# Kernel optimization log

Hardware: AMD Instinct MI355X
Metric: run time of the kernel (lower is better)

Reference implementation:

```python
import jax, jax.numpy as jnp
import numpy as np

DIM = 1024
NUM_HEADS = 16
HEAD_DIM = DIM // NUM_HEADS
EPS_NORM = 1e-12  # F.normalize eps
EPS_LN = 1e-5     # nn.LayerNorm eps


def setup_inputs() -> dict:
    key = jax.random.key(0)
    ks = jax.random.split(key, 6)
    x = jax.random.normal(ks[0], (4, 2048, DIM), dtype=jnp.float32)
    # LayerNorm params
    ln_w = jnp.ones((DIM,), jnp.float32)
    ln_b = jnp.zeros((DIM,), jnp.float32)
    # qkv: xavier_uniform on weight [3D, D], zero bias
    limit = float(np.sqrt(6.0 / (DIM + 3 * DIM)))
    qkv_w = jax.random.uniform(ks[1], (3 * DIM, DIM), jnp.float32, -limit, limit)
    qkv_b = jnp.zeros((3 * DIM,), jnp.float32)
    # out_proj: normal std=0.02, zero bias
    out_w = 0.02 * jax.random.normal(ks[2], (DIM, DIM), dtype=jnp.float32)
    out_b = jnp.zeros((DIM,), jnp.float32)
    return {"x": x, "ln_w": ln_w, "ln_b": ln_b, "qkv_w": qkv_w,
            "qkv_b": qkv_b, "out_w": out_w, "out_b": out_b}


def reference(x, ln_w, ln_b, qkv_w, qkv_b, out_w, out_b):
    B, N, D = x.shape
    # pre-LayerNorm
    mu = jnp.mean(x, axis=-1, keepdims=True)
    var = jnp.mean(jnp.square(x - mu), axis=-1, keepdims=True)
    h = (x - mu) / jnp.sqrt(var + EPS_LN) * ln_w + ln_b
    # QKV projection (torch Linear: y = h @ W^T + b)
    qkv = h @ qkv_w.T + qkv_b                     # [B, N, 3D]
    qkv = qkv.reshape(B, N, 3, NUM_HEADS, HEAD_DIM)
    q, k, v = (jnp.transpose(qkv[:, :, i], (0, 2, 1, 3)) for i in range(3))  # [B,H,N,hd]
    # per-head L2 normalize (F.normalize semantics: x / max(||x||, eps))
    q = q / jnp.maximum(jnp.linalg.norm(q, axis=-1, keepdims=True), EPS_NORM)
    k = k / jnp.maximum(jnp.linalg.norm(k, axis=-1, keepdims=True), EPS_NORM)
    scale = HEAD_DIM ** 0.5
    attn = jnp.einsum('bhqd,bhkd->bhqk', q, k) * scale
    attn = jax.nn.softmax(attn, axis=-1)
    out = jnp.einsum('bhqk,bhkd->bhqd', attn, v)  # [B,H,N,hd]
    out = jnp.transpose(out, (0, 2, 1, 3)).reshape(B, N, D)
    return x + out @ out_w.T + out_b
```

## Files before the change

### kernel.cpp

```cpp
#include <hip/hip_runtime.h>
#include <math.h>

constexpr int D     = 1024;
constexpr int NH    = 16;
constexpr int HD    = 64;
constexpr int SEQ   = 2048;
constexpr int BATCH = 4;
constexpr int NTOK  = BATCH * SEQ;

typedef short s16x8 __attribute__((ext_vector_type(8)));
typedef short s16x4 __attribute__((ext_vector_type(4)));
typedef float f32x4 __attribute__((ext_vector_type(4)));
typedef unsigned short u16;
typedef unsigned int   u32;

#if __has_builtin(__builtin_amdgcn_exp2f)
#define EXP2(x) __builtin_amdgcn_exp2f(x)
#else
#define EXP2(x) exp2f(x)
#endif

__device__ __forceinline__ short f2bf(float f) {
    unsigned u = __float_as_uint(f);
    unsigned r = (u + 0x7FFFu + ((u >> 16) & 1u)) >> 16;
    return (short)r;
}
__device__ __forceinline__ float bf2f(u16 s) {
    return __uint_as_float(((unsigned)s) << 16);
}

__device__ __forceinline__ u32 pack_bf16_pair(float f0, float f1) {
    u32 a = __float_as_uint(f1) + 0x8000u;
    u32 b = __float_as_uint(f0) + 0x8000u;
    return __builtin_amdgcn_perm(a, b, 0x07060302u);
}

__device__ __forceinline__ void async_lds16(const void* g, void* l) {
    __builtin_amdgcn_global_load_lds(
        (const __attribute__((address_space(1))) unsigned int*)g,
        (__attribute__((address_space(3))) unsigned int*)l, 16, 0, 0);
}

__device__ __forceinline__ float block_reduce_sum(float v, float* red) {
    int lane = threadIdx.x & 63, wid = threadIdx.x >> 6;
    #pragma unroll
    for (int off = 32; off > 0; off >>= 1) v += __shfl_down(v, off, 64);
    if (lane == 0) red[wid] = v;
    __syncthreads();
    float r = red[0] + red[1] + red[2] + red[3];
    __syncthreads();
    return r;
}

__global__ __launch_bounds__(256) void ln_kernel(const float* __restrict__ x,
                                                 const float* __restrict__ w,
                                                 const float* __restrict__ b,
                                                 u16* __restrict__ h) {
    __shared__ float red[4];
    int row = blockIdx.x;
    const float* xr = x + (size_t)row * D;
    int t = threadIdx.x;
    float v[4];
    float s = 0.f;
    #pragma unroll
    for (int i = 0; i < 4; i++) { v[i] = xr[t + 256 * i]; s += v[i]; }
    float mean = block_reduce_sum(s, red) * (1.0f / 1024.0f);
    float ss = 0.f;
    #pragma unroll
    for (int i = 0; i < 4; i++) { float d = v[i] - mean; ss += d * d; }
    float var = block_reduce_sum(ss, red) * (1.0f / 1024.0f);
    float rstd = rsqrtf(var + 1e-5f);
    u16* hr = h + (size_t)row * D;
    #pragma unroll
    for (int i = 0; i < 4; i++) {
        int c = t + 256 * i;
        hr[c] = (u16)f2bf((v[i] - mean) * rstd * w[c] + b[c]);
    }
}

__global__ __launch_bounds__(256) void cast_kernel(const float* __restrict__ in,
                                                   u16* __restrict__ out, int n) {
    int i = (blockIdx.x * 256 + threadIdx.x) * 4;
    if (i >= n) return;
    float4 f = *(const float4*)(in + i);
    s16x4 o4;
    o4[0] = f2bf(f.x); o4[1] = f2bf(f.y); o4[2] = f2bf(f.z); o4[3] = f2bf(f.w);
    *(s16x4*)(out + i) = o4;
}

template <typename OutT, bool RES>
__global__ __launch_bounds__(256) void gemm_bf16(const u16* __restrict__ A,
                                                 const u16* __restrict__ B,
                                                 const float* __restrict__ bias,
                                                 const float* __restrict__ R,
                                                 OutT* __restrict__ C,
                                                 int M, int N, int K) {
    __shared__ u16 As[128 * 32];
    __shared__ u16 Bs[128 * 32];
    int tid = threadIdx.x, wave = tid >> 6, lane = tid & 63;
    int quad = lane >> 4, l16 = lane & 15;
    int wm = (wave & 1) * 64, wn = (wave >> 1) * 64;
    int rowBase = blockIdx.y * 128, colBase = blockIdx.x * 128;

    int srow = lane >> 2;
    int sk8  = (lane & 3) * 8;

    f32x4 acc[4][4];
    #pragma unroll
    for (int i = 0; i < 4; i++)
        #pragma unroll
        for (int j = 0; j < 4; j++)
            acc[i][j] = (f32x4){0.f, 0.f, 0.f, 0.f};

    for (int k0 = 0; k0 < K; k0 += 32) {
        __syncthreads();
        #pragma unroll
        for (int i = 0; i < 2; i++) {
            int r = wave * 32 + i * 16;
            const u16* ga = A + (size_t)(rowBase + r + srow) * K + k0 + sk8;
            async_lds16(ga, &As[r * 32]);
            const u16* gb = B + (size_t)(colBase + r + srow) * K + k0 + sk8;
            async_lds16(gb, &Bs[r * 32]);
        }
        __syncthreads();

        s16x8 af[4], bfr[4];
        #pragma unroll
        for (int t = 0; t < 4; t++) {
            af[t]  = *(const s16x8*)&As[(wm + t * 16 + l16) * 32 + quad * 8];
            bfr[t] = *(const s16x8*)&Bs[(wn + t * 16 + l16) * 32 + quad * 8];
        }
        #pragma unroll
        for (int mt = 0; mt < 4; mt++)
            #pragma unroll
            for (int nt = 0; nt < 4; nt++)
                acc[mt][nt] = __builtin_amdgcn_mfma_f32_16x16x32_bf16(
                    af[mt], bfr[nt], acc[mt][nt], 0, 0, 0);
    }

    #pragma unroll
    for (int mt = 0; mt < 4; mt++) {
        #pragma unroll
        for (int nt = 0; nt < 4; nt++) {
            int gm0 = rowBase + wm + mt * 16 + quad * 4;
            int gn  = colBase + wn + nt * 16 + l16;
            float bv = bias[gn];
            #pragma unroll
            for (int r = 0; r < 4; r++) {
                int gm = gm0 + r;
                float val = acc[mt][nt][r] + bv;
                if (RES) val += R[(size_t)gm * N + gn];
                if constexpr (sizeof(OutT) == 2)
                    C[(size_t)gm * N + gn] = (OutT)f2bf(val);
                else
                    C[(size_t)gm * N + gn] = val;
            }
        }
    }
}

__global__ __launch_bounds__(256) void knorm_kernel(u16* __restrict__ qkv) {
    int gw = (blockIdx.x * 256 + threadIdx.x) >> 6;
    int lane = threadIdx.x & 63;
    int row = gw / NH, hh = gw - row * NH;
    u16* kp = qkv + (size_t)row * 3072 + 1024 + hh * 64;

    float kv = bf2f(kp[lane]);
    float s = kv * kv;
    #pragma unroll
    for (int off = 32; off > 0; off >>= 1) s += __shfl_down(s, off, 64);
    s = __shfl(s, 0, 64);
    kp[lane] = (u16)f2bf(kv / fmaxf(sqrtf(s), 1e-12f));
}

__global__ __launch_bounds__(256, 2) void mha_kernel(const u16* __restrict__ qkv,
                                                     u16* __restrict__ out) {
    __shared__ u16 Ks[64 * 64];
    constexpr int VS = 68;
    __shared__ u16 Vt[64 * VS];

    int bh = blockIdx.x >> 3;
    int qt = blockIdx.x & 7;
    int b  = bh >> 4, h = bh & 15;
    int tid = threadIdx.x;
    int wave = tid >> 6, lane = tid & 63;
    int quad = lane >> 4, l16 = lane & 15;

    const size_t rs = 3072;
    constexpr float SCL = 11.5415605f;

    s16x8 aq[4][2];
    #pragma unroll
    for (int rt = 0; rt < 4; rt++) {
        const u16* qb = qkv + ((size_t)(b * SEQ) + qt * 256 + wave * 64 + rt * 16 + l16) * rs + h * 64;
        s16x8 r0 = *(const s16x8*)(qb + quad * 8);
        s16x8 r1 = *(const s16x8*)(qb + 32 + quad * 8);
        float f0[8], f1[8], ss = 0.f;
        #pragma unroll
        for (int i = 0; i < 8; i++) { f0[i] = bf2f((u16)r0[i]); ss = fmaf(f0[i], f0[i], ss); }
        #pragma unroll
        for (int i = 0; i < 8; i++) { f1[i] = bf2f((u16)r1[i]); ss = fmaf(f1[i], f1[i], ss); }
        ss += __shfl_xor(ss, 16, 64);
        ss += __shfl_xor(ss, 32, 64);
        float inv = SCL / fmaxf(sqrtf(ss), 1e-12f);
        #pragma unroll
        for (int i = 0; i < 8; i++) {
            aq[rt][0][i] = f2bf(f0[i] * inv);
            aq[rt][1][i] = f2bf(f1[i] * inv);
        }
    }

    const f32x4 cinit = {-SCL, -SCL, -SCL, -SCL};
    f32x4 o2[4][4];
    #pragma unroll
    for (int rt = 0; rt < 4; rt++)
        #pragma unroll
        for (int ht = 0; ht < 4; ht++) o2[rt][ht] = (f32x4){0.f, 0.f, 0.f, 0.f};
    float lsum[4] = {0.f, 0.f, 0.f, 0.f};

    int skey = tid >> 2, c4 = tid & 3;
    int ksw  = skey & 7;
    int vp2 = tid >> 3, dc = (tid & 7) * 8;
    const u16* kglob  = qkv + ((size_t)(b * SEQ) + skey) * rs + 1024 + h * 64 + c4 * 16;
    const u16* vglob0 = qkv + ((size_t)(b * SEQ) + 2 * vp2) * rs + 2048 + h * 64 + dc;
    u16* kdst0 = &Ks[skey * 64 + ((2 * c4)     ^ ksw) * 8];
    u16* kdst1 = &Ks[skey * 64 + ((2 * c4 + 1) ^ ksw) * 8];
    u32* vt32 = (u32*)&Vt[0];

    s16x8 kr0 = ((const s16x8*)kglob)[0];
    s16x8 kr1 = ((const s16x8*)kglob)[1];
    s16x8 vr0 = *(const s16x8*)(vglob0);
    s16x8 vr1 = *(const s16x8*)(vglob0 + rs);

    int swz = l16 & 7;

    for (int kb = 0; kb < SEQ / 64; kb++) {
        __syncthreads();
        *(s16x8*)kdst0 = kr0;
        *(s16x8*)kdst1 = kr1;
        #pragma unroll
        for (int i = 0; i < 8; i++) {
            u32 pk = (u32)(u16)vr0[i] | ((u32)(u16)vr1[i] << 16);
            vt32[(dc + i) * (VS / 2) + vp2] = pk;
        }
        __syncthreads();

        if (kb < SEQ / 64 - 1) {
            const u16* kp = kglob + (size_t)(kb + 1) * 64 * rs;
            const u16* vp = vglob0 + (size_t)(kb + 1) * 64 * rs;
            kr0 = ((const s16x8*)kp)[0];
            kr1 = ((const s16x8*)kp)[1];
            vr0 = *(const s16x8*)(vp);
            vr1 = *(const s16x8*)(vp + rs);
        }

        s16x4 pfr[4][4];
        float sum16[4] = {0.f, 0.f, 0.f, 0.f};
        #pragma unroll
        for (int t = 0; t < 4; t++) {
            const u16* krow = &Ks[(t * 16 + l16) * 64];
            s16x8 bk0 = *(const s16x8*)(krow + ((0 + quad) ^ swz) * 8);
            s16x8 bk1 = *(const s16x8*)(krow + ((4 + quad) ^ swz) * 8);
            #pragma unroll
            for (int rt = 0; rt < 4; rt++) {
                f32x4 s = cinit;
                s = __builtin_amdgcn_mfma_f32_16x16x32_bf16(bk0, aq[rt][0], s, 0, 0, 0);
                s = __builtin_amdgcn_mfma_f32_16x16x32_bf16(bk1, aq[rt][1], s, 0, 0, 0);
                float p0 = EXP2(s[0]);
                float p1 = EXP2(s[1]);
                float p2 = EXP2(s[2]);
                float p3 = EXP2(s[3]);
                sum16[rt] += (p0 + p1) + (p2 + p3);
                uint2 pk2;
                pk2.x = pack_bf16_pair(p0, p1);
                pk2.y = pack_bf16_pair(p2, p3);
                pfr[rt][t] = __builtin_bit_cast(s16x4, pk2);
            }
        }
        #pragma unroll
        for (int rt = 0; rt < 4; rt++) {
            float s16v = sum16[rt];
            s16v += __shfl_xor(s16v, 16, 64);
            s16v += __shfl_xor(s16v, 32, 64);
            lsum[rt] += s16v;
        }

        #pragma unroll
        for (int pr = 0; pr < 2; pr++) {
            int tA = pr * 2, tB = pr * 2 + 1;
            #pragma unroll
            for (int ht = 0; ht < 4; ht++) {
                const u16* vrow = &Vt[(ht * 16 + l16) * VS];
                s16x4 va = *(const s16x4*)(vrow + tA * 16 + quad * 4);
                s16x4 vb = *(const s16x4*)(vrow + tB * 16 + quad * 4);
                s16x8 vfr = __builtin_shufflevector(va, vb, 0, 1, 2, 3, 4, 5, 6, 7);
                #pragma unroll
                for (int rt = 0; rt < 4; rt++) {
                    s16x8 bp = __builtin_shufflevector(pfr[rt][tA], pfr[rt][tB],
                                                       0, 1, 2, 3, 4, 5, 6, 7);
                    o2[rt][ht] = __builtin_amdgcn_mfma_f32_16x16x32_bf16(
                        vfr, bp, o2[rt][ht], 0, 0, 0);
                }
            }
        }
    }

    #pragma unroll
    for (int rt = 0; rt < 4; rt++) {
        float inv = 1.0f / lsum[rt];
        int orow = b * SEQ + qt * 256 + wave * 64 + rt * 16 + l16;
        u16* op = out + (size_t)orow * D + h * 64 + quad * 4;
        #pragma unroll
        for (int ht = 0; ht < 4; ht++) {
            f32x4 v = o2[rt][ht];
            u32 lo = pack_bf16_pair(v[0] * inv, v[1] * inv);
            u32 hi = pack_bf16_pair(v[2] * inv, v[3] * inv);
            uint2 pk = {lo, hi};
            *(uint2*)(op + ht * 16) = pk;
        }
    }
}

extern "C" void kernel_launch(void* const* d_in, const int* in_sizes, int n_in,
                              void* d_out, int out_size, void* d_ws, size_t ws_size,
                              hipStream_t stream) {
    const float* x     = (const float*)d_in[0];
    const float* ln_w  = (const float*)d_in[1];
    const float* ln_b  = (const float*)d_in[2];
    const float* qkv_w = (const float*)d_in[3];
    const float* qkv_b = (const float*)d_in[4];
    const float* out_w = (const float*)d_in[5];
    const float* out_b = (const float*)d_in[6];
    float* y = (float*)d_out;

    char* ws = (char*)d_ws;
    u16* qkv = (u16*)ws;
    u16* h   = (u16*)(ws + (size_t)48 * 1024 * 1024);
    u16* wq  = (u16*)(ws + (size_t)64 * 1024 * 1024);
    u16* wo  = (u16*)(ws + (size_t)70 * 1024 * 1024);
    u16* attn_out = h;

    ln_kernel<<<NTOK, 256, 0, stream>>>(x, ln_w, ln_b, h);
    cast_kernel<<<(3 * D * D) / 1024, 256, 0, stream>>>(qkv_w, wq, 3 * D * D);
    cast_kernel<<<(D * D) / 1024, 256, 0, stream>>>(out_w, wo, D * D);

    {
        dim3 grid(3 * D / 128, NTOK / 128);
        gemm_bf16<u16, false><<<grid, 256, 0, stream>>>(h, wq, qkv_b, nullptr, qkv,
                                                        NTOK, 3 * D, D);
    }

    knorm_kernel<<<NTOK * NH / 4, 256, 0, stream>>>(qkv);

    mha_kernel<<<BATCH * NH * (SEQ / 256), 256, 0, stream>>>(qkv, attn_out);

    {
        dim3 grid(D / 128, NTOK / 128);
        gemm_bf16<float, true><<<grid, 256, 0, stream>>>(attn_out, wo, out_b, x, y,
                                                         NTOK, D, D);
    }
}
```

Measured before the change: 312.3 us.

## Fuse K normalization into QKV GEMM epilogue and compute softmax sums via MFMA

Removes the separate knorm kernel by L2-normalizing K head slices inside the QKV GEMM epilogue, which saves one read-modify-write pass over K. In the attention kernel, the row sums of the softmax are now accumulated with an extra MFMA against a ones vector instead of scalar adds and cross-lane shuffles, and the P operands are packed once per pair. The block index mapping is also changed so consecutive blocks cover different heads for the same query tile. The trade-offs are extra MFMA work, row sums accumulated from bf16-rounded probabilities, and extra shuffles in the GEMM epilogue.

```diff
diff --git a/kernel.cpp b/kernel.cpp
--- a/kernel.cpp
+++ b/kernel.cpp
@@ -88,7 +88,7 @@
     *(s16x4*)(out + i) = o4;
 }
 
-template <typename OutT, bool RES>
+template <typename OutT, bool RES, bool NORMK>
 __global__ __launch_bounds__(256) void gemm_bf16(const u16* __restrict__ A,
                                                  const u16* __restrict__ B,
                                                  const float* __restrict__ bias,
@@ -138,39 +138,53 @@
                     af[mt], bfr[nt], acc[mt][nt], 0, 0, 0);
     }
 
+    bool normk = NORMK && (colBase + wn) >= 1024 && (colBase + wn) < 2048;
+
     #pragma unroll
     for (int mt = 0; mt < 4; mt++) {
+        float vals[4][4];
         #pragma unroll
         for (int nt = 0; nt < 4; nt++) {
+            int gn = colBase + wn + nt * 16 + l16;
+            float bv = bias[gn];
+            #pragma unroll
+            for (int r = 0; r < 4; r++) {
+                float val = acc[mt][nt][r] + bv;
+                if (RES) {
+                    int gm = rowBase + wm + mt * 16 + quad * 4 + r;
+                    val += R[(size_t)gm * N + gn];
+                }
+                vals[nt][r] = val;
+            }
+        }
+        if (normk) {
+            #pragma unroll
+            for (int r = 0; r < 4; r++) {
+                float ssq = 0.f;
+                #pragma unroll
+                for (int nt = 0; nt < 4; nt++) ssq = fmaf(vals[nt][r], vals[nt][r], ssq);
+                ssq += __shfl_xor(ssq, 1, 64);
+                ssq += __shfl_xor(ssq, 2, 64);
+                ssq += __shfl_xor(ssq, 4, 64);
+                ssq += __shfl_xor(ssq, 8, 64);
+                float inv = 1.0f / fmaxf(sqrtf(ssq), 1e-12f);
+                #pragma unroll
+                for (int nt = 0; nt < 4; nt++) vals[nt][r] *= inv;
+            }
+        }
+        #pragma unroll
+        for (int nt = 0; nt < 4; nt++) {
+            int gn = colBase + wn + nt * 16 + l16;
             int gm0 = rowBase + wm + mt * 16 + quad * 4;
-            int gn  = colBase + wn + nt * 16 + l16;
-            float bv = bias[gn];
             #pragma unroll
             for (int r = 0; r < 4; r++) {
-                int gm = gm0 + r;
-                float val = acc[mt][nt][r] + bv;
-                if (RES) val += R[(size_t)gm * N + gn];
                 if constexpr (sizeof(OutT) == 2)
-                    C[(size_t)gm * N + gn] = (OutT)f2bf(val);
+                    C[(size_t)(gm0 + r) * N + gn] = (OutT)f2bf(vals[nt][r]);
                 else
-                    C[(size_t)gm * N + gn] = val;
-            }
-        }
-    }
-}
-
-__global__ __launch_bounds__(256) void knorm_kernel(u16* __restrict__ qkv) {
-    int gw = (blockIdx.x * 256 + threadIdx.x) >> 6;
-    int lane = threadIdx.x & 63;
-    int row = gw / NH, hh = gw - row * NH;
-    u16* kp = qkv + (size_t)row * 3072 + 1024 + hh * 64;
-
-    float kv = bf2f(kp[lane]);
-    float s = kv * kv;
-    #pragma unroll
-    for (int off = 32; off > 0; off >>= 1) s += __shfl_down(s, off, 64);
-    s = __shfl(s, 0, 64);
-    kp[lane] = (u16)f2bf(kv / fmaxf(sqrtf(s), 1e-12f));
+                    C[(size_t)(gm0 + r) * N + gn] = vals[nt][r];
+            }
+        }
+    }
 }
 
 __global__ __launch_bounds__(256, 2) void mha_kernel(const u16* __restrict__ qkv,
@@ -179,8 +193,8 @@
     constexpr int VS = 68;
     __shared__ u16 Vt[64 * VS];
 
-    int bh = blockIdx.x >> 3;
-    int qt = blockIdx.x & 7;
+    int bh = blockIdx.x & 63;
+    int qt = blockIdx.x >> 6;
     int b  = bh >> 4, h = bh & 15;
     int tid = threadIdx.x;
     int wave = tid >> 6, lane = tid & 63;
@@ -212,11 +226,16 @@
 
     const f32x4 cinit = {-SCL, -SCL, -SCL, -SCL};
     f32x4 o2[4][4];
-    #pragma unroll
-    for (int rt = 0; rt < 4; rt++)
+    f32x4 osum[4];
+    #pragma unroll
+    for (int rt = 0; rt < 4; rt++) {
         #pragma unroll
         for (int ht = 0; ht < 4; ht++) o2[rt][ht] = (f32x4){0.f, 0.f, 0.f, 0.f};
-    float lsum[4] = {0.f, 0.f, 0.f, 0.f};
+        osum[rt] = (f32x4){0.f, 0.f, 0.f, 0.f};
+    }
+    s16x8 ones;
+    #pragma unroll
+    for (int i = 0; i < 8; i++) ones[i] = (short)0x3F80;
 
     int skey = tid >> 2, c4 = tid & 3;
     int ksw  = skey & 7;
@@ -255,7 +274,6 @@
         }
 
         s16x4 pfr[4][4];
-        float sum16[4] = {0.f, 0.f, 0.f, 0.f};
         #pragma unroll
         for (int t = 0; t < 4; t++) {
             const u16* krow = &Ks[(t * 16 + l16) * 64];
@@ -266,28 +284,21 @@
                 f32x4 s = cinit;
                 s = __builtin_amdgcn_mfma_f32_16x16x32_bf16(bk0, aq[rt][0], s, 0, 0, 0);
                 s = __builtin_amdgcn_mfma_f32_16x16x32_bf16(bk1, aq[rt][1], s, 0, 0, 0);
-                float p0 = EXP2(s[0]);
-                float p1 = EXP2(s[1]);
-                float p2 = EXP2(s[2]);
-                float p3 = EXP2(s[3]);
-                sum16[rt] += (p0 + p1) + (p2 + p3);
                 uint2 pk2;
-                pk2.x = pack_bf16_pair(p0, p1);
-                pk2.y = pack_bf16_pair(p2, p3);
+                pk2.x = pack_bf16_pair(EXP2(s[0]), EXP2(s[1]));
+                pk2.y = pack_bf16_pair(EXP2(s[2]), EXP2(s[3]));
                 pfr[rt][t] = __builtin_bit_cast(s16x4, pk2);
             }
-        }
-        #pragma unroll
-        for (int rt = 0; rt < 4; rt++) {
-            float s16v = sum16[rt];
-            s16v += __shfl_xor(s16v, 16, 64);
-            s16v += __shfl_xor(s16v, 32, 64);
-            lsum[rt] += s16v;
         }
 
         #pragma unroll
         for (int pr = 0; pr < 2; pr++) {
             int tA = pr * 2, tB = pr * 2 + 1;
+            s16x8 bp[4];
+            #pragma unroll
+            for (int rt = 0; rt < 4; rt++)
+                bp[rt] = __builtin_shufflevector(pfr[rt][tA], pfr[rt][tB],
+                                                 0, 1, 2, 3, 4, 5, 6, 7);
             #pragma unroll
             for (int ht = 0; ht < 4; ht++) {
                 const u16* vrow = &Vt[(ht * 16 + l16) * VS];
@@ -295,19 +306,20 @@
                 s16x4 vb = *(const s16x4*)(vrow + tB * 16 + quad * 4);
                 s16x8 vfr = __builtin_shufflevector(va, vb, 0, 1, 2, 3, 4, 5, 6, 7);
                 #pragma unroll
-                for (int rt = 0; rt < 4; rt++) {
-                    s16x8 bp = __builtin_shufflevector(pfr[rt][tA], pfr[rt][tB],
-                                                       0, 1, 2, 3, 4, 5, 6, 7);
+                for (int rt = 0; rt < 4; rt++)
                     o2[rt][ht] = __builtin_amdgcn_mfma_f32_16x16x32_bf16(
-                        vfr, bp, o2[rt][ht], 0, 0, 0);
-                }
-            }
+                        vfr, bp[rt], o2[rt][ht], 0, 0, 0);
+            }
+            #pragma unroll
+            for (int rt = 0; rt < 4; rt++)
+                osum[rt] = __builtin_amdgcn_mfma_f32_16x16x32_bf16(
+                    ones, bp[rt], osum[rt], 0, 0, 0);
         }
     }
 
     #pragma unroll
     for (int rt = 0; rt < 4; rt++) {
-        float inv = 1.0f / lsum[rt];
+        float inv = 1.0f / osum[rt][0];
         int orow = b * SEQ + qt * 256 + wave * 64 + rt * 16 + l16;
         u16* op = out + (size_t)orow * D + h * 64 + quad * 4;
         #pragma unroll
@@ -346,17 +358,15 @@
 
     {
         dim3 grid(3 * D / 128, NTOK / 128);
-        gemm_bf16<u16, false><<<grid, 256, 0, stream>>>(h, wq, qkv_b, nullptr, qkv,
-                                                        NTOK, 3 * D, D);
-    }
-
-    knorm_kernel<<<NTOK * NH / 4, 256, 0, stream>>>(qkv);
+        gemm_bf16<u16, false, true><<<grid, 256, 0, stream>>>(h, wq, qkv_b, nullptr,
+                                                              qkv, NTOK, 3 * D, D);
+    }
 
     mha_kernel<<<BATCH * NH * (SEQ / 256), 256, 0, stream>>>(qkv, attn_out);
 
     {
         dim3 grid(D / 128, NTOK / 128);
-        gemm_bf16<float, true><<<grid, 256, 0, stream>>>(attn_out, wo, out_b, x, y,
-                                                         NTOK, D, D);
-    }
-}
+        gemm_bf16<float, true, false><<<grid, 256, 0, stream>>>(attn_out, wo, out_b,
+                                                                x, y, NTOK, D, D);
+    }
+}
```

Result: faster. 284.9 us (-8.8%).
